# Optimization experiments

Measured on AMD Instinct MI355X. Metric: run time of the kernel, lower is better.

The kernel has to match this reference:

```python
import jax, jax.numpy as jnp
import numpy as np
import math

B, S, D = 16, 1024, 512
ALPHA = 1.0
DIRECTION = 'fw'


def masked_softmax(vec, mask):
    # faithful to the torch helper: multiply-by-mask, max-shift, exp, re-mask, normalize
    masked_vec = vec * mask
    max_vec = jnp.max(masked_vec, axis=2, keepdims=True)
    exps = jnp.exp(masked_vec - max_vec)
    masked_exps = exps * mask
    masked_sums = jnp.sum(masked_exps, axis=2, keepdims=True)
    masked_sums = masked_sums + (masked_sums == 0).astype(vec.dtype)
    return masked_exps / (masked_sums + 1e-20)


def setup_inputs() -> dict:
    key = jax.random.key(0)
    kq, kk, kv, km = jax.random.split(key, 4)
    q = jax.random.normal(kq, (B, S, D), dtype=jnp.float32)
    k = jax.random.normal(kk, (B, S, D), dtype=jnp.float32)
    v = jax.random.normal(kv, (B, S, D), dtype=jnp.float32)
    rep_mask = jax.random.randint(km, (B, S, 1), 0, 2, dtype=jnp.int32)
    return {"q": q, "k": k, "v": v, "rep_mask": rep_mask}


def reference(q, k, v, rep_mask):
    seq_len = q.shape[1]
    scale = jnp.asarray(math.sqrt(D), dtype=q.dtype)
    attention = jnp.einsum('bqd,bkd->bqk', q, k) / scale  # [B,S,S]

    ones = jnp.ones((seq_len, seq_len), dtype=q.dtype)
    if DIRECTION == 'fw':
        dir_mask = jnp.tril(ones, k=-1)
    else:
        dir_mask = jnp.triu(ones, k=1)

    rm = rep_mask.astype(q.dtype)                     # [B,S,1]
    rep = rm * jnp.swapaxes(rm, 1, 2)                 # [B,S,S]

    idx = jnp.arange(seq_len)
    dis_mask = -jnp.abs(idx[:, None] - idx[None, :]).astype(q.dtype)  # [S,S]

    mask = rep * dir_mask[None]                       # [B,S,S]
    attention = attention + ALPHA * dis_mask[None]
    attention = masked_softmax(attention, mask)
    out = jnp.einsum('bqk,bkd->bqd', attention, v)
    return (out, attention)
```

## Files before the change

kernel.cpp:

```cpp
#include <hip/hip_runtime.h>
#include <cstdint>

#define B_ 16
#define S_ 1024
#define D_ 512
#define TILE 128
#define BK 32
#define PITCH 36

typedef float f32x4 __attribute__((ext_vector_type(4)));
typedef short s16x8 __attribute__((ext_vector_type(8)));
typedef unsigned short u16;
typedef unsigned int u32;

__device__ __forceinline__ u16 f2bf(float f) {
    u32 u = __builtin_bit_cast(u32, f);
    u += 0x7FFFu + ((u >> 16) & 1u);
    return (u16)(u >> 16);
}


#define GLD16(g, l) __builtin_amdgcn_global_load_lds( \
    (const __attribute__((address_space(1))) u32*)(g), \
    (__attribute__((address_space(3))) u32*)(l), 16, 0, 0)

__global__ __launch_bounds__(256) void cvt_kernel(const float* __restrict__ src,
                                                  u16* __restrict__ dst) {
    int i = (blockIdx.x * 256 + threadIdx.x) * 8;
    float4 a = *(const float4*)(src + i);
    float4 b = *(const float4*)(src + i + 4);
    union { ushort4 h[2]; s16x8 v; } r;
    r.h[0] = make_ushort4(f2bf(a.x), f2bf(a.y), f2bf(a.z), f2bf(a.w));
    r.h[1] = make_ushort4(f2bf(b.x), f2bf(b.y), f2bf(b.z), f2bf(b.w));
    *(s16x8*)(dst + i) = r.v;
}

#define TP 66
__global__ __launch_bounds__(256) void trv_kernel(const float* __restrict__ v,
                                                  u16* __restrict__ vt) {
    const int d0 = blockIdx.x * 64, j0 = blockIdx.y * 64, b = blockIdx.z;
    __shared__ u16 t[64 * TP];
    const int tid = threadIdx.x;
    const int tj = tid >> 2;
    const int td = (tid & 3) * 16;
    const float* src = v + ((size_t)b * S_ + j0 + tj) * D_ + d0 + td;
#pragma unroll
    for (int e = 0; e < 4; ++e) {
        float4 a = *(const float4*)(src + e * 4);
        *(ushort4*)(t + tj * TP + td + e * 4) =
            make_ushort4(f2bf(a.x), f2bf(a.y), f2bf(a.z), f2bf(a.w));
    }
    __syncthreads();
    const int dd = tid >> 2;
    const int jj = (tid & 3) * 16;
    u16* dstp = vt + ((size_t)b * D_ + d0 + dd) * S_ + j0 + jj;
    u16 tmp[16];
#pragma unroll
    for (int e = 0; e < 16; ++e) tmp[e] = t[(jj + e) * TP + dd];
    *(s16x8*)dstp = *(s16x8*)tmp;
    *(s16x8*)(dstp + 8) = *(s16x8*)(tmp + 8);
}

__device__ __forceinline__ s16x8 frag_swz(const u16* lds, int row, int colbyte) {
    int off = row * 128 + (colbyte ^ ((row & 7) << 4));
    return *(const s16x8*)((const char*)lds + off);
}

__device__ __forceinline__ void gemm_body(const u16* ag, const u16* bg, int lda, int ldb,
                                          int nk, u16* lA, u16* lB, f32x4 acc[4][4],
                                          int tid) {
    const int lane = tid & 63, wid = tid >> 6;
    const int l8 = lane >> 3, l7 = lane & 7;
    const int cswz = (l7 ^ l8) * 8;
    const u16* ga[4];
    const u16* gb[4];
#pragma unroll
    for (int q2 = 0; q2 < 4; ++q2) {
        int seg = wid * 4 + q2;
        int row = seg * 8 + l8;
        ga[q2] = ag + (size_t)row * lda + cswz;
        gb[q2] = bg + (size_t)row * ldb + cswz;
    }
    const int wr = (wid >> 1) * 64, wc = (wid & 1) * 64;
    const int r15 = lane & 15;
    const int cb = (lane >> 4) * 16;

    for (int kk = 0; kk < nk; kk += 64) {
#pragma unroll
        for (int q2 = 0; q2 < 4; ++q2) {
            int seg = wid * 4 + q2;
            GLD16(ga[q2] + kk, lA + seg * 512);
            GLD16(gb[q2] + kk, lB + seg * 512);
        }
        __syncthreads();
#pragma unroll
        for (int ks = 0; ks < 2; ++ks) {
            s16x8 af[4], bf4[4];
#pragma unroll
            for (int m = 0; m < 4; ++m) af[m] = frag_swz(lA, wr + m * 16 + r15, ks * 64 + cb);
#pragma unroll
            for (int n = 0; n < 4; ++n) bf4[n] = frag_swz(lB, wc + n * 16 + r15, ks * 64 + cb);
#pragma unroll
            for (int m = 0; m < 4; ++m)
#pragma unroll
                for (int n = 0; n < 4; ++n)
                    acc[m][n] = __builtin_amdgcn_mfma_f32_16x16x32_bf16(af[m], bf4[n], acc[m][n], 0, 0, 0);
        }
        __syncthreads();
    }
}

__global__ __launch_bounds__(256) void qk2_kernel(const u16* __restrict__ Qb,
                                                  const u16* __restrict__ Kb,
                                                  float* __restrict__ attn) {
    const int kt = blockIdx.x, qt = blockIdx.y, b = blockIdx.z;
    if (kt > qt) return;
    __shared__ u16 lA[128 * 64];
    __shared__ u16 lB[128 * 64];
    const int tid = threadIdx.x, lane = tid & 63, wid = tid >> 6;
    f32x4 acc[4][4] = {};
    gemm_body(Qb + ((size_t)b * S_ + (size_t)qt * 128) * D_,
              Kb + ((size_t)b * S_ + (size_t)kt * 128) * D_,
              D_, D_, D_, lA, lB, acc, tid);
    const float scale = 0.04419417382415922f;
    const int wr = (wid >> 1) * 64, wc = (wid & 1) * 64;
    const int r15 = lane & 15, rr = (lane >> 4) * 4;
    size_t base = ((size_t)b * S_ + (size_t)qt * 128) * S_ + (size_t)kt * 128;
#pragma unroll
    for (int m = 0; m < 4; ++m)
#pragma unroll
        for (int n = 0; n < 4; ++n)
#pragma unroll
            for (int r = 0; r < 4; ++r)
                attn[base + (size_t)(wr + m * 16 + rr + r) * S_ + wc + n * 16 + r15] =
                    acc[m][n][r] * scale;
}

__global__ __launch_bounds__(256) void pv2_kernel(const u16* __restrict__ Pb,
                                                  const u16* __restrict__ Vt,
                                                  float* __restrict__ out) {
    const int dt = blockIdx.x, qt = blockIdx.y, b = blockIdx.z;
    __shared__ u16 lA[128 * 64];
    __shared__ u16 lB[128 * 64];
    const int tid = threadIdx.x, lane = tid & 63, wid = tid >> 6;
    f32x4 acc[4][4] = {};
    gemm_body(Pb + ((size_t)b * S_ + (size_t)qt * 128) * S_,
              Vt + ((size_t)b * D_ + (size_t)dt * 128) * S_,
              S_, S_, (qt + 1) * 128, lA, lB, acc, tid);
    const int wr = (wid >> 1) * 64, wc = (wid & 1) * 64;
    const int r15 = lane & 15, rr = (lane >> 4) * 4;
    size_t base = ((size_t)b * S_ + (size_t)qt * 128) * D_ + (size_t)dt * 128;
#pragma unroll
    for (int m = 0; m < 4; ++m)
#pragma unroll
        for (int n = 0; n < 4; ++n)
#pragma unroll
            for (int r = 0; r < 4; ++r)
                out[base + (size_t)(wr + m * 16 + rr + r) * D_ + wc + n * 16 + r15] =
                    acc[m][n][r];
}

__global__ __launch_bounds__(256) void sm_kernel(const int* __restrict__ rep_mask,
                                                 float* __restrict__ attn,
                                                 u16* __restrict__ pb) {
    const int i = blockIdx.x, b = blockIdx.y;
    const int tid = threadIdx.x;
    const int lane = tid & 63, wid = tid >> 6;
    float* row = attn + ((size_t)b * S_ + i) * S_;
    const int* rm = rep_mask + (size_t)b * S_;
    __shared__ float red[8];

    const int mi = rm[i];
    const int j0 = tid * 4;
    int4 m4 = ((const int4*)rm)[tid];
    float4 lv = make_float4(0.f, 0.f, 0.f, 0.f);
    if (mi != 0 && j0 < i) lv = *(const float4*)(row + j0);

    const int mv[4] = {m4.x, m4.y, m4.z, m4.w};
    const float lf[4] = {lv.x, lv.y, lv.z, lv.w};
    float vec[4];
    bool val[4];
    float mymax = 0.0f;
#pragma unroll
    for (int e = 0; e < 4; ++e) {
        int j = j0 + e;
        val[e] = (mi != 0) && (j < i) && (mv[e] != 0);
        vec[e] = lf[e] - (float)(i - j);
        if (val[e]) mymax = fmaxf(mymax, vec[e]);
    }
#pragma unroll
    for (int off = 32; off > 0; off >>= 1) mymax = fmaxf(mymax, __shfl_down(mymax, off));
    if (lane == 0) red[wid] = mymax;
    __syncthreads();
    const float m = fmaxf(fmaxf(red[0], red[1]), fmaxf(red[2], red[3]));

    float ex[4];
    float mysum = 0.0f;
#pragma unroll
    for (int e = 0; e < 4; ++e) {
        ex[e] = val[e] ? expf(vec[e] - m) : 0.0f;
        mysum += ex[e];
    }
#pragma unroll
    for (int off = 32; off > 0; off >>= 1) mysum += __shfl_down(mysum, off);
    if (lane == 0) red[4 + wid] = mysum;
    __syncthreads();
    const float ssum = red[4] + red[5] + red[6] + red[7];
    const float denom = ssum + (ssum == 0.0f ? 1.0f : 0.0f) + 1e-20f;
    const float inv = 1.0f / denom;
    float4 o = make_float4(ex[0] * inv, ex[1] * inv, ex[2] * inv, ex[3] * inv);
    *(float4*)(row + j0) = o;
    if (pb != nullptr && j0 <= (i | 127)) {
        u16* pr = pb + ((size_t)b * S_ + i) * S_ + j0;
        *(ushort4*)pr = make_ushort4(f2bf(o.x), f2bf(o.y), f2bf(o.z), f2bf(o.w));
    }
}


union Frag { s16x8 v; uint2 u[2]; };

__device__ __forceinline__ s16x8 load_frag(const u16* lds, int row, int kq) {
    Frag f;
    const u16* p = lds + row * PITCH + kq;
    f.u[0] = *(const uint2*)p;
    f.u[1] = *(const uint2*)(p + 4);
    return f.v;
}

__device__ __forceinline__ void stage_granule(u16* lds, const float* src, int ldsrc, int g) {
    int row = g >> 2;
    int c8 = (g & 3) * 8;
    const float4* s = (const float4*)(src + (size_t)row * ldsrc + c8);
    float4 x0 = s[0], x1 = s[1];
    *(ushort4*)(lds + row * PITCH + c8) =
        make_ushort4(f2bf(x0.x), f2bf(x0.y), f2bf(x0.z), f2bf(x0.w));
    *(ushort4*)(lds + row * PITCH + c8 + 4) =
        make_ushort4(f2bf(x1.x), f2bf(x1.y), f2bf(x1.z), f2bf(x1.w));
}

__global__ __launch_bounds__(256) void qk_kernel(const float* __restrict__ q,
                                                 const float* __restrict__ k,
                                                 float* __restrict__ attn) {
    const int kt = blockIdx.x, qt = blockIdx.y, b = blockIdx.z;
    if (kt > qt) return;
    __shared__ u16 lA[TILE * PITCH];
    __shared__ u16 lB[TILE * PITCH];
    const int tid = threadIdx.x;
    const int lane = tid & 63;
    const int wid = tid >> 6;
    const int wr = (wid >> 1) * 64, wc = (wid & 1) * 64;
    const int r15 = lane & 15, kq = (lane >> 4) * 8;
    const float* qb = q + ((size_t)b * S_ + (size_t)qt * TILE) * D_;
    const float* kb = k + ((size_t)b * S_ + (size_t)kt * TILE) * D_;
    f32x4 acc[4][4] = {};
    for (int kk = 0; kk < D_; kk += BK) {
        __syncthreads();
        stage_granule(lA, qb + kk, D_, tid);
        stage_granule(lA, qb + kk, D_, tid + 256);
        stage_granule(lB, kb + kk, D_, tid);
        stage_granule(lB, kb + kk, D_, tid + 256);
        __syncthreads();
        s16x8 af[4], bf[4];
#pragma unroll
        for (int m = 0; m < 4; ++m) af[m] = load_frag(lA, wr + m * 16 + r15, kq);
#pragma unroll
        for (int n = 0; n < 4; ++n) bf[n] = load_frag(lB, wc + n * 16 + r15, kq);
#pragma unroll
        for (int m = 0; m < 4; ++m)
#pragma unroll
            for (int n = 0; n < 4; ++n)
                acc[m][n] = __builtin_amdgcn_mfma_f32_16x16x32_bf16(af[m], bf[n], acc[m][n], 0, 0, 0);
    }
    const float scale = 0.04419417382415922f;
    size_t base = ((size_t)b * S_ + (size_t)qt * TILE) * S_ + (size_t)kt * TILE;
    const int rr = (lane >> 4) * 4;
#pragma unroll
    for (int m = 0; m < 4; ++m)
#pragma unroll
        for (int n = 0; n < 4; ++n)
#pragma unroll
            for (int r = 0; r < 4; ++r)
                attn[base + (size_t)(wr + m * 16 + rr + r) * S_ + wc + n * 16 + r15] =
                    acc[m][n][r] * scale;
}

__global__ __launch_bounds__(256) void pv_kernel(const float* __restrict__ attn,
                                                 const float* __restrict__ v,
                                                 float* __restrict__ out) {
    const int dt = blockIdx.x, qt = blockIdx.y, b = blockIdx.z;
    __shared__ u16 lP[TILE * PITCH];
    __shared__ u16 lV[TILE * PITCH];
    const int tid = threadIdx.x;
    const int lane = tid & 63;
    const int wid = tid >> 6;
    const int wr = (wid >> 1) * 64, wc = (wid & 1) * 64;
    const int r15 = lane & 15, kq = (lane >> 4) * 8;
    const float* pb = attn + ((size_t)b * S_ + (size_t)qt * TILE) * S_;
    const float* vb = v + (size_t)b * S_ * D_ + (size_t)dt * TILE;
    const int vd0 = (tid & 31) * 4;
    const int vj0 = (tid >> 5) * 4;
    f32x4 acc[4][4] = {};
    const int nk = (qt + 1) * TILE;
    for (int kk = 0; kk < nk; kk += BK) {
        __syncthreads();
        stage_granule(lP, pb + kk, S_, tid);
        stage_granule(lP, pb + kk, S_, tid + 256);
        {
            const float* vs = vb + (size_t)(kk + vj0) * D_ + vd0;
            float4 r0 = *(const float4*)vs;
            float4 r1 = *(const float4*)(vs + D_);
            float4 r2 = *(const float4*)(vs + 2 * D_);
            float4 r3 = *(const float4*)(vs + 3 * D_);
            *(ushort4*)(lV + (vd0 + 0) * PITCH + vj0) = make_ushort4(f2bf(r0.x), f2bf(r1.x), f2bf(r2.x), f2bf(r3.x));
            *(ushort4*)(lV + (vd0 + 1) * PITCH + vj0) = make_ushort4(f2bf(r0.y), f2bf(r1.y), f2bf(r2.y), f2bf(r3.y));
            *(ushort4*)(lV + (vd0 + 2) * PITCH + vj0) = make_ushort4(f2bf(r0.z), f2bf(r1.z), f2bf(r2.z), f2bf(r3.z));
            *(ushort4*)(lV + (vd0 + 3) * PITCH + vj0) = make_ushort4(f2bf(r0.w), f2bf(r1.w), f2bf(r2.w), f2bf(r3.w));
        }
        __syncthreads();
        s16x8 af[4], bf[4];
#pragma unroll
        for (int m = 0; m < 4; ++m) af[m] = load_frag(lP, wr + m * 16 + r15, kq);
#pragma unroll
        for (int n = 0; n < 4; ++n) bf[n] = load_frag(lV, wc + n * 16 + r15, kq);
#pragma unroll
        for (int m = 0; m < 4; ++m)
#pragma unroll
            for (int n = 0; n < 4; ++n)
                acc[m][n] = __builtin_amdgcn_mfma_f32_16x16x32_bf16(af[m], bf[n], acc[m][n], 0, 0, 0);
    }
    size_t base = ((size_t)b * S_ + (size_t)qt * TILE) * D_ + (size_t)dt * TILE;
    const int rr = (lane >> 4) * 4;
#pragma unroll
    for (int m = 0; m < 4; ++m)
#pragma unroll
        for (int n = 0; n < 4; ++n)
#pragma unroll
            for (int r = 0; r < 4; ++r)
                out[base + (size_t)(wr + m * 16 + rr + r) * D_ + wc + n * 16 + r15] =
                    acc[m][n][r];
}

extern "C" void kernel_launch(void* const* d_in, const int* in_sizes, int n_in,
                              void* d_out, int out_size, void* d_ws, size_t ws_size,
                              hipStream_t stream) {
    const float* q = (const float*)d_in[0];
    const float* k = (const float*)d_in[1];
    const float* v = (const float*)d_in[2];
    const int* rep = (const int*)d_in[3];
    float* out = (float*)d_out;
    float* attn = out + (size_t)B_ * S_ * D_;

    const size_t nqk = (size_t)B_ * S_ * D_;
    const size_t need = 3 * nqk * sizeof(u16);
    if (ws_size >= need) {
        u16* Qb = (u16*)d_ws;
        u16* Kb = Qb + nqk;
        u16* Vt = Kb + nqk;
        u16* Pb = (u16*)d_ws;
        cvt_kernel<<<nqk / (8 * 256), 256, 0, stream>>>(q, Qb);
        cvt_kernel<<<nqk / (8 * 256), 256, 0, stream>>>(k, Kb);
        trv_kernel<<<dim3(D_ / 64, S_ / 64, B_), 256, 0, stream>>>(v, Vt);
        qk2_kernel<<<dim3(8, 8, B_), 256, 0, stream>>>(Qb, Kb, attn);
        sm_kernel<<<dim3(S_, B_), 256, 0, stream>>>(rep, attn, Pb);
        pv2_kernel<<<dim3(4, 8, B_), 256, 0, stream>>>(Pb, Vt, out);
    } else {
        qk_kernel<<<dim3(S_ / TILE, S_ / TILE, B_), 256, 0, stream>>>(q, k, attn);
        sm_kernel<<<dim3(S_, B_), 256, 0, stream>>>(rep, attn, nullptr);
        pv_kernel<<<dim3(D_ / TILE, S_ / TILE, B_), 256, 0, stream>>>(attn, v, out);
    }
}
```

Baseline: 104.3 us.

## Fuse QK^T with masked softmax and read fp32 probabilities directly in PV

Replaces the separate QK GEMM and row-softmax kernels with one kernel. Each block owns 32 query rows, converts Q to bf16 in LDS, streams K, and does the masked softmax with in-register and cross-wave max/sum reductions, writing final probabilities straight to the attention output. The PV kernel now reads fp32 probabilities and converts them to bf16 while staging, which removes the bf16 P buffer, the Q conversion kernel and one round trip of the score matrix through memory. Blocks are remapped so that batches group by XCD and the heavier causal tiles are scheduled first. The cost is lower per-block parallelism and a large LDS footprint, plus conversion work inside the PV loop.

```diff
diff --git a/kernel.cpp b/kernel.cpp
--- a/kernel.cpp
+++ b/kernel.cpp
@@ -18,7 +18,6 @@
     u += 0x7FFFu + ((u >> 16) & 1u);
     return (u16)(u >> 16);
 }
-
 
 #define GLD16(g, l) __builtin_amdgcn_global_load_lds( \
     (const __attribute__((address_space(1))) u32*)(g), \
@@ -61,159 +60,250 @@
     *(s16x8*)(dstp + 8) = *(s16x8*)(tmp + 8);
 }
 
+__global__ __launch_bounds__(512, 2) void fused_qksm(const float* __restrict__ q,
+                                                     const u16* __restrict__ Kb,
+                                                     const int* __restrict__ rep,
+                                                     float* __restrict__ attn) {
+    const int bid = blockIdx.x;
+    const int xcd = bid & 7, w = bid >> 3;
+    const int b = xcd * 2 + (w & 1);
+    const int qc = 31 - (w >> 1);
+    const int i0 = qc * 32;
+    const int ncolt = (qc >> 2) + 1;
+    const int ncol = ncolt * 128;
+
+    __shared__ u16 lQ[32 * 512];
+    __shared__ u16 lK[1024 * 32];
+    __shared__ int lrep[1024];
+    __shared__ float lred[8][32][2];
+    __shared__ float lrs[32][2];
+
+    const int tid = threadIdx.x, lane = tid & 63, wid = tid >> 6;
+    const int r15 = lane & 15, g4 = lane >> 4;
+
+    {
+        int2 rv = ((const int2*)(rep + (size_t)b * S_))[tid];
+        lrep[tid * 2] = rv.x;
+        lrep[tid * 2 + 1] = rv.y;
+    }
+    {
+        const float* qg = q + ((size_t)b * S_ + i0) * D_;
+#pragma unroll
+        for (int e = 0; e < 4; ++e) {
+            int G = e * 512 + tid;
+            int i = G >> 6, c8 = G & 63;
+            const float* src = qg + i * D_ + c8 * 8;
+            float4 x0 = *(const float4*)src;
+            float4 x1 = *(const float4*)(src + 4);
+            union { ushort4 h[2]; s16x8 v; } rr;
+            rr.h[0] = make_ushort4(f2bf(x0.x), f2bf(x0.y), f2bf(x0.z), f2bf(x0.w));
+            rr.h[1] = make_ushort4(f2bf(x1.x), f2bf(x1.y), f2bf(x1.z), f2bf(x1.w));
+            int unit = c8 ^ (i & 7);
+            *(s16x8*)(lQ + i * 512 + unit * 8) = rr.v;
+        }
+    }
+    __syncthreads();
+
+    const u16* kbase = Kb + (size_t)b * S_ * D_;
+    f32x4 acc[2][8] = {};
+
+    for (int kk = 0; kk < 512; kk += 32) {
+        for (int t = 0; t < ncolt; ++t) {
+            int ud = t * 512 + tid;
+            int p = ud >> 3, u = ud & 7;
+            int lu = u ^ (p & 7);
+            int j = p * 2 + (lu >> 2);
+            int k16 = lu & 3;
+            GLD16(kbase + (size_t)j * D_ + kk + k16 * 8, lK + t * 4096 + wid * 512);
+        }
+        __syncthreads();
+        if (wid < ncolt) {
+            s16x8 av[2], bv[8];
+            int c8 = (kk >> 3) + g4;
+#pragma unroll
+            for (int rf = 0; rf < 2; ++rf) {
+                int i = rf * 16 + r15;
+                av[rf] = *(const s16x8*)(lQ + i * 512 + (c8 ^ (i & 7)) * 8);
+            }
+#pragma unroll
+            for (int cf = 0; cf < 8; ++cf) {
+                int j = wid * 128 + cf * 16 + r15;
+                int p = j >> 1;
+                int lu = (j & 1) * 4 + g4;
+                bv[cf] = *(const s16x8*)(lK + p * 64 + (lu ^ (p & 7)) * 8);
+            }
+#pragma unroll
+            for (int rf = 0; rf < 2; ++rf)
+#pragma unroll
+                for (int cf = 0; cf < 8; ++cf)
+                    acc[rf][cf] = __builtin_amdgcn_mfma_f32_16x16x32_bf16(av[rf], bv[cf], acc[rf][cf], 0, 0, 0);
+        }
+        __syncthreads();
+    }
+
+    const float scale = 0.04419417382415922f;
+    int mj[8];
+#pragma unroll
+    for (int cf = 0; cf < 8; ++cf) mj[cf] = lrep[wid * 128 + cf * 16 + r15];
+    int mi_[2][4];
+#pragma unroll
+    for (int rf = 0; rf < 2; ++rf)
+#pragma unroll
+        for (int r = 0; r < 4; ++r) mi_[rf][r] = lrep[i0 + rf * 16 + g4 * 4 + r];
+
+    float pm[2][4], ps[2][4];
+#pragma unroll
+    for (int rf = 0; rf < 2; ++rf)
+#pragma unroll
+        for (int r = 0; r < 4; ++r) {
+            const int i = i0 + rf * 16 + g4 * 4 + r;
+            const int im = mi_[rf][r];
+            float m = 0.0f;
+#pragma unroll
+            for (int cf = 0; cf < 8; ++cf) {
+                int j = wid * 128 + cf * 16 + r15;
+                if (im && (j < i) && mj[cf])
+                    m = fmaxf(m, acc[rf][cf][r] * scale - (float)(i - j));
+            }
+            float s = 0.0f;
+#pragma unroll
+            for (int cf = 0; cf < 8; ++cf) {
+                int j = wid * 128 + cf * 16 + r15;
+                if (im && (j < i) && mj[cf])
+                    s += __expf(acc[rf][cf][r] * scale - (float)(i - j) - m);
+            }
+#pragma unroll
+            for (int off = 1; off < 16; off <<= 1) {
+                float om = __shfl_xor(m, off);
+                float os = __shfl_xor(s, off);
+                float M = fmaxf(m, om);
+                s = s * __expf(m - M) + os * __expf(om - M);
+                m = M;
+            }
+            pm[rf][r] = m;
+            ps[rf][r] = s;
+        }
+    if (r15 == 0) {
+#pragma unroll
+        for (int rf = 0; rf < 2; ++rf)
+#pragma unroll
+            for (int r = 0; r < 4; ++r) {
+                int rowl = rf * 16 + g4 * 4 + r;
+                lred[wid][rowl][0] = pm[rf][r];
+                lred[wid][rowl][1] = ps[rf][r];
+            }
+    }
+    __syncthreads();
+    if (tid < 32) {
+        float M = 0.0f, S = 0.0f;
+#pragma unroll
+        for (int w2 = 0; w2 < 8; ++w2) M = fmaxf(M, lred[w2][tid][0]);
+#pragma unroll
+        for (int w2 = 0; w2 < 8; ++w2) S += lred[w2][tid][1] * __expf(lred[w2][tid][0] - M);
+        float denom = (S == 0.0f ? 1.0f : S) + 1e-20f;
+        lrs[tid][0] = M;
+        lrs[tid][1] = 1.0f / denom;
+    }
+    __syncthreads();
+
+    float* arow = attn + ((size_t)b * S_ + i0) * S_;
+#pragma unroll
+    for (int rf = 0; rf < 2; ++rf)
+#pragma unroll
+        for (int r = 0; r < 4; ++r) {
+            const int il = rf * 16 + g4 * 4 + r;
+            const int i = i0 + il;
+            const int im = mi_[rf][r];
+            const float M = lrs[il][0], inv = lrs[il][1];
+#pragma unroll
+            for (int cf = 0; cf < 8; ++cf) {
+                int j = wid * 128 + cf * 16 + r15;
+                float pv = 0.0f;
+                if (im && (j < i) && mj[cf])
+                    pv = __expf(acc[rf][cf][r] * scale - (float)(i - j) - M) * inv;
+                arow[(size_t)il * S_ + j] = pv;
+            }
+        }
+}
+
 __device__ __forceinline__ s16x8 frag_swz(const u16* lds, int row, int colbyte) {
     int off = row * 128 + (colbyte ^ ((row & 7) << 4));
     return *(const s16x8*)((const char*)lds + off);
 }
 
-__device__ __forceinline__ void gemm_body(const u16* ag, const u16* bg, int lda, int ldb,
-                                          int nk, u16* lA, u16* lB, f32x4 acc[4][4],
-                                          int tid) {
-    const int lane = tid & 63, wid = tid >> 6;
-    const int l8 = lane >> 3, l7 = lane & 7;
-    const int cswz = (l7 ^ l8) * 8;
-    const u16* ga[4];
-    const u16* gb[4];
-#pragma unroll
-    for (int q2 = 0; q2 < 4; ++q2) {
-        int seg = wid * 4 + q2;
-        int row = seg * 8 + l8;
-        ga[q2] = ag + (size_t)row * lda + cswz;
-        gb[q2] = bg + (size_t)row * ldb + cswz;
-    }
-    const int wr = (wid >> 1) * 64, wc = (wid & 1) * 64;
-    const int r15 = lane & 15;
-    const int cb = (lane >> 4) * 16;
-
-    for (int kk = 0; kk < nk; kk += 64) {
-#pragma unroll
-        for (int q2 = 0; q2 < 4; ++q2) {
-            int seg = wid * 4 + q2;
-            GLD16(ga[q2] + kk, lA + seg * 512);
-            GLD16(gb[q2] + kk, lB + seg * 512);
-        }
-        __syncthreads();
-#pragma unroll
-        for (int ks = 0; ks < 2; ++ks) {
-            s16x8 af[4], bf4[4];
-#pragma unroll
-            for (int m = 0; m < 4; ++m) af[m] = frag_swz(lA, wr + m * 16 + r15, ks * 64 + cb);
-#pragma unroll
-            for (int n = 0; n < 4; ++n) bf4[n] = frag_swz(lB, wc + n * 16 + r15, ks * 64 + cb);
-#pragma unroll
-            for (int m = 0; m < 4; ++m)
-#pragma unroll
-                for (int n = 0; n < 4; ++n)
-                    acc[m][n] = __builtin_amdgcn_mfma_f32_16x16x32_bf16(af[m], bf4[n], acc[m][n], 0, 0, 0);
-        }
-        __syncthreads();
-    }
-}
-
-__global__ __launch_bounds__(256) void qk2_kernel(const u16* __restrict__ Qb,
-                                                  const u16* __restrict__ Kb,
-                                                  float* __restrict__ attn) {
-    const int kt = blockIdx.x, qt = blockIdx.y, b = blockIdx.z;
-    if (kt > qt) return;
+__global__ __launch_bounds__(256) void pv3_kernel(const float* __restrict__ attn,
+                                                  const u16* __restrict__ Vt,
+                                                  float* __restrict__ out) {
+    const int bid = blockIdx.x;
+    const int xcd = bid & 7, w = bid >> 3;
+    const int b = xcd * 2 + (w & 1);
+    const int r_ = w >> 1;
+    const int dt = r_ & 3, qt = 7 - (r_ >> 2);
+
     __shared__ u16 lA[128 * 64];
     __shared__ u16 lB[128 * 64];
     const int tid = threadIdx.x, lane = tid & 63, wid = tid >> 6;
+    const int l8 = lane >> 3, l7 = lane & 7;
+    const int cswz = (l7 ^ l8) * 8;
+
+    const float* ag = attn + ((size_t)b * S_ + (size_t)qt * 128) * S_;
+    const u16* bg = Vt + ((size_t)b * D_ + (size_t)dt * 128) * S_;
+    const u16* gb[4];
+#pragma unroll
+    for (int q2 = 0; q2 < 4; ++q2) {
+        int seg = wid * 4 + q2;
+        gb[q2] = bg + (size_t)(seg * 8 + l8) * S_ + cswz;
+    }
+    const int au = tid & 7;
+    const int ar0 = (tid >> 3) * 4;
+
     f32x4 acc[4][4] = {};
-    gemm_body(Qb + ((size_t)b * S_ + (size_t)qt * 128) * D_,
-              Kb + ((size_t)b * S_ + (size_t)kt * 128) * D_,
-              D_, D_, D_, lA, lB, acc, tid);
-    const float scale = 0.04419417382415922f;
+    const int nk = (qt + 1) * 128;
     const int wr = (wid >> 1) * 64, wc = (wid & 1) * 64;
-    const int r15 = lane & 15, rr = (lane >> 4) * 4;
-    size_t base = ((size_t)b * S_ + (size_t)qt * 128) * S_ + (size_t)kt * 128;
+    const int r15 = lane & 15, cb = (lane >> 4) * 16;
+
+    for (int kk = 0; kk < nk; kk += 64) {
+#pragma unroll
+        for (int q2 = 0; q2 < 4; ++q2)
+            GLD16(gb[q2] + kk, lB + (wid * 4 + q2) * 512);
+#pragma unroll
+        for (int rr = 0; rr < 4; ++rr) {
+            int row = ar0 + rr;
+            const float* src = ag + (size_t)row * S_ + kk + au * 8;
+            float4 x0 = *(const float4*)src;
+            float4 x1 = *(const float4*)(src + 4);
+            union { ushort4 h[2]; s16x8 v; } rv;
+            rv.h[0] = make_ushort4(f2bf(x0.x), f2bf(x0.y), f2bf(x0.z), f2bf(x0.w));
+            rv.h[1] = make_ushort4(f2bf(x1.x), f2bf(x1.y), f2bf(x1.z), f2bf(x1.w));
+            *(s16x8*)(lA + row * 64 + (au ^ (row & 7)) * 8) = rv.v;
+        }
+        __syncthreads();
+        s16x8 af[4], bf4[4];
+#pragma unroll
+        for (int ks = 0; ks < 2; ++ks) {
+#pragma unroll
+            for (int m = 0; m < 4; ++m) af[m] = frag_swz(lA, wr + m * 16 + r15, ks * 64 + cb);
+#pragma unroll
+            for (int n = 0; n < 4; ++n) bf4[n] = frag_swz(lB, wc + n * 16 + r15, ks * 64 + cb);
+#pragma unroll
+            for (int m = 0; m < 4; ++m)
+#pragma unroll
+                for (int n = 0; n < 4; ++n)
+                    acc[m][n] = __builtin_amdgcn_mfma_f32_16x16x32_bf16(af[m], bf4[n], acc[m][n], 0, 0, 0);
+        }
+        __syncthreads();
+    }
+
+    size_t base = ((size_t)b * S_ + (size_t)qt * 128) * D_ + (size_t)dt * 128;
+    const int rr2 = (lane >> 4) * 4;
 #pragma unroll
     for (int m = 0; m < 4; ++m)
 #pragma unroll
         for (int n = 0; n < 4; ++n)
 #pragma unroll
             for (int r = 0; r < 4; ++r)
-                attn[base + (size_t)(wr + m * 16 + rr + r) * S_ + wc + n * 16 + r15] =
-                    acc[m][n][r] * scale;
-}
-
-__global__ __launch_bounds__(256) void pv2_kernel(const u16* __restrict__ Pb,
-                                                  const u16* __restrict__ Vt,
-                                                  float* __restrict__ out) {
-    const int dt = blockIdx.x, qt = blockIdx.y, b = blockIdx.z;
-    __shared__ u16 lA[128 * 64];
-    __shared__ u16 lB[128 * 64];
-    const int tid = threadIdx.x, lane = tid & 63, wid = tid >> 6;
-    f32x4 acc[4][4] = {};
-    gemm_body(Pb + ((size_t)b * S_ + (size_t)qt * 128) * S_,
-              Vt + ((size_t)b * D_ + (size_t)dt * 128) * S_,
-              S_, S_, (qt + 1) * 128, lA, lB, acc, tid);
-    const int wr = (wid >> 1) * 64, wc = (wid & 1) * 64;
-    const int r15 = lane & 15, rr = (lane >> 4) * 4;
-    size_t base = ((size_t)b * S_ + (size_t)qt * 128) * D_ + (size_t)dt * 128;
-#pragma unroll
-    for (int m = 0; m < 4; ++m)
-#pragma unroll
-        for (int n = 0; n < 4; ++n)
-#pragma unroll
-            for (int r = 0; r < 4; ++r)
-                out[base + (size_t)(wr + m * 16 + rr + r) * D_ + wc + n * 16 + r15] =
+                out[base + (size_t)(wr + m * 16 + rr2 + r) * D_ + wc + n * 16 + r15] =
                     acc[m][n][r];
-}
-
-__global__ __launch_bounds__(256) void sm_kernel(const int* __restrict__ rep_mask,
-                                                 float* __restrict__ attn,
-                                                 u16* __restrict__ pb) {
-    const int i = blockIdx.x, b = blockIdx.y;
-    const int tid = threadIdx.x;
-    const int lane = tid & 63, wid = tid >> 6;
-    float* row = attn + ((size_t)b * S_ + i) * S_;
-    const int* rm = rep_mask + (size_t)b * S_;
-    __shared__ float red[8];
-
-    const int mi = rm[i];
-    const int j0 = tid * 4;
-    int4 m4 = ((const int4*)rm)[tid];
-    float4 lv = make_float4(0.f, 0.f, 0.f, 0.f);
-    if (mi != 0 && j0 < i) lv = *(const float4*)(row + j0);
-
-    const int mv[4] = {m4.x, m4.y, m4.z, m4.w};
-    const float lf[4] = {lv.x, lv.y, lv.z, lv.w};
-    float vec[4];
-    bool val[4];
-    float mymax = 0.0f;
-#pragma unroll
-    for (int e = 0; e < 4; ++e) {
-        int j = j0 + e;
-        val[e] = (mi != 0) && (j < i) && (mv[e] != 0);
-        vec[e] = lf[e] - (float)(i - j);
-        if (val[e]) mymax = fmaxf(mymax, vec[e]);
-    }
-#pragma unroll
-    for (int off = 32; off > 0; off >>= 1) mymax = fmaxf(mymax, __shfl_down(mymax, off));
-    if (lane == 0) red[wid] = mymax;
-    __syncthreads();
-    const float m = fmaxf(fmaxf(red[0], red[1]), fmaxf(red[2], red[3]));
-
-    float ex[4];
-    float mysum = 0.0f;
-#pragma unroll
-    for (int e = 0; e < 4; ++e) {
-        ex[e] = val[e] ? expf(vec[e] - m) : 0.0f;
-        mysum += ex[e];
-    }
-#pragma unroll
-    for (int off = 32; off > 0; off >>= 1) mysum += __shfl_down(mysum, off);
-    if (lane == 0) red[4 + wid] = mysum;
-    __syncthreads();
-    const float ssum = red[4] + red[5] + red[6] + red[7];
-    const float denom = ssum + (ssum == 0.0f ? 1.0f : 0.0f) + 1e-20f;
-    const float inv = 1.0f / denom;
-    float4 o = make_float4(ex[0] * inv, ex[1] * inv, ex[2] * inv, ex[3] * inv);
-    *(float4*)(row + j0) = o;
-    if (pb != nullptr && j0 <= (i | 127)) {
-        u16* pr = pb + ((size_t)b * S_ + i) * S_ + j0;
-        *(ushort4*)pr = make_ushort4(f2bf(o.x), f2bf(o.y), f2bf(o.z), f2bf(o.w));
-    }
 }
 
 
@@ -282,6 +372,53 @@
             for (int r = 0; r < 4; ++r)
                 attn[base + (size_t)(wr + m * 16 + rr + r) * S_ + wc + n * 16 + r15] =
                     acc[m][n][r] * scale;
+}
+
+__global__ __launch_bounds__(256) void sm_kernel(const int* __restrict__ rep_mask,
+                                                 float* __restrict__ attn) {
+    const int i = blockIdx.x, b = blockIdx.y;
+    const int tid = threadIdx.x;
+    const int lane = tid & 63, wid = tid >> 6;
+    float* row = attn + ((size_t)b * S_ + i) * S_;
+    const int* rm = rep_mask + (size_t)b * S_;
+    __shared__ float red[8];
+    const int mi = rm[i];
+    const int j0 = tid * 4;
+    int4 m4 = ((const int4*)rm)[tid];
+    float4 lv = make_float4(0.f, 0.f, 0.f, 0.f);
+    if (mi != 0 && j0 < i) lv = *(const float4*)(row + j0);
+    const int mv[4] = {m4.x, m4.y, m4.z, m4.w};
+    const float lf[4] = {lv.x, lv.y, lv.z, lv.w};
+    float vec[4];
+    bool val[4];
+    float mymax = 0.0f;
+#pragma unroll
+    for (int e = 0; e < 4; ++e) {
+        int j = j0 + e;
+        val[e] = (mi != 0) && (j < i) && (mv[e] != 0);
+        vec[e] = lf[e] - (float)(i - j);
+        if (val[e]) mymax = fmaxf(mymax, vec[e]);
+    }
+#pragma unroll
+    for (int off = 32; off > 0; off >>= 1) mymax = fmaxf(mymax, __shfl_down(mymax, off));
+    if (lane == 0) red[wid] = mymax;
+    __syncthreads();
+    const float m = fmaxf(fmaxf(red[0], red[1]), fmaxf(red[2], red[3]));
+    float ex[4];
+    float mysum = 0.0f;
+#pragma unroll
+    for (int e = 0; e < 4; ++e) {
+        ex[e] = val[e] ? expf(vec[e] - m) : 0.0f;
+        mysum += ex[e];
+    }
+#pragma unroll
+    for (int off = 32; off > 0; off >>= 1) mysum += __shfl_down(mysum, off);
+    if (lane == 0) red[4 + wid] = mysum;
+    __syncthreads();
+    const float ssum = red[4] + red[5] + red[6] + red[7];
+    const float denom = ssum + (ssum == 0.0f ? 1.0f : 0.0f) + 1e-20f;
+    const float inv = 1.0f / denom;
+    *(float4*)(row + j0) = make_float4(ex[0] * inv, ex[1] * inv, ex[2] * inv, ex[3] * inv);
 }
 
 __global__ __launch_bounds__(256) void pv_kernel(const float* __restrict__ attn,
@@ -351,21 +488,17 @@
     float* attn = out + (size_t)B_ * S_ * D_;
 
     const size_t nqk = (size_t)B_ * S_ * D_;
-    const size_t need = 3 * nqk * sizeof(u16);
+    const size_t need = 2 * nqk * sizeof(u16);
     if (ws_size >= need) {
-        u16* Qb = (u16*)d_ws;
-        u16* Kb = Qb + nqk;
+        u16* Kb = (u16*)d_ws;
         u16* Vt = Kb + nqk;
-        u16* Pb = (u16*)d_ws;
-        cvt_kernel<<<nqk / (8 * 256), 256, 0, stream>>>(q, Qb);
         cvt_kernel<<<nqk / (8 * 256), 256, 0, stream>>>(k, Kb);
         trv_kernel<<<dim3(D_ / 64, S_ / 64, B_), 256, 0, stream>>>(v, Vt);
-        qk2_kernel<<<dim3(8, 8, B_), 256, 0, stream>>>(Qb, Kb, attn);
-        sm_kernel<<<dim3(S_, B_), 256, 0, stream>>>(rep, attn, Pb);
-        pv2_kernel<<<dim3(4, 8, B_), 256, 0, stream>>>(Pb, Vt, out);
+        fused_qksm<<<512, 512, 0, stream>>>(q, Kb, rep, attn);
+        pv3_kernel<<<512, 256, 0, stream>>>(attn, Vt, out);
     } else {
         qk_kernel<<<dim3(S_ / TILE, S_ / TILE, B_), 256, 0, stream>>>(q, k, attn);
-        sm_kernel<<<dim3(S_, B_), 256, 0, stream>>>(rep, attn, nullptr);
+        sm_kernel<<<dim3(S_, B_), 256, 0, stream>>>(rep, attn);
         pv_kernel<<<dim3(D_ / TILE, S_ / TILE, B_), 256, 0, stream>>>(attn, v, out);
     }
 }
```

Result: no change. 105.9 us (+1.5%).
